# Optimization experiments

Measured on AMD Instinct MI355X. Metric: run time of the kernel, lower is better.

Reference implementation:

```python
import jax, jax.numpy as jnp
import numpy as np

N = 16384
B = 64
VOCAB = 100
L0 = 128
RADIUS = 8.0
BOX = 50.0


def setup_inputs() -> dict:
    key = jax.random.key(0)
    ks = jax.random.split(key, 8)
    z = jax.random.randint(ks[0], (N,), 0, VOCAB, dtype=jnp.int32)
    batch = jnp.sort(jax.random.randint(ks[1], (N,), 0, B, dtype=jnp.int64))
    pos = jax.random.uniform(ks[2], (N, 3), dtype=jnp.float32) * BOX
    emb = jax.random.normal(ks[3], (VOCAB, L0), dtype=jnp.float32)
    w1 = jax.random.normal(ks[4], (L0, 64), dtype=jnp.float32) * (1.0 / np.sqrt(L0))
    b1 = jnp.zeros((64,), dtype=jnp.float32)
    w2 = jax.random.normal(ks[5], (64, 1), dtype=jnp.float32) * (1.0 / 8.0)
    b2 = jnp.zeros((1,), dtype=jnp.float32)
    return {"z": z, "batch": batch, "pos": pos, "emb": emb,
            "w1": w1, "b1": b1, "w2": w2, "b2": b2}


def _radius_graph_mask(pos, batch, r):
    # Brute-force radius graph (what torch_cluster does without grid binning):
    # pairwise squared distances, thresholded, same-graph, no self-loops.
    # Returns a dense [N, N] bool adjacency mask (fixed shape, jit-friendly).
    sq = jnp.sum(pos * pos, axis=-1)                       # [N]
    d2 = sq[:, None] + sq[None, :] - 2.0 * (pos @ pos.T)   # [N, N]
    same_graph = batch[:, None] == batch[None, :]
    not_self = ~jnp.eye(pos.shape[0], dtype=bool)
    return (d2 < r * r) & same_graph & not_self


def reference(z, batch, pos, emb, w1, b1, w2, b2):
    nodes = emb[z]                                         # [N, L0] embedding lookup
    adj = _radius_graph_mask(pos, batch, RADIUS)           # [N, N] bool
    h = jax.nn.silu(nodes @ w1 + b1)                       # [N, 64]
    out = h @ w2 + b2                                      # [N, 1]
    return out, adj
```

## Files before the change

kernel.cpp:

```cpp
#include <hip/hip_runtime.h>
#include <hip/hip_bf16.h>
#include <math.h>

#define N_NODES 16384
#define TI 64
#define TJ 1024

typedef float vf4 __attribute__((ext_vector_type(4)));

__global__ __launch_bounds__(256) void mlp_kernel(const int* __restrict__ z,
                                                  const float* __restrict__ emb,
                                                  const float* __restrict__ w1,
                                                  const float* __restrict__ b1,
                                                  const float* __restrict__ w2,
                                                  const float* __restrict__ b2,
                                                  const int* __restrict__ batch32,
                                                  int* __restrict__ flag,
                                                  float* __restrict__ out) {
    if (blockIdx.x == 0) {
        __shared__ int dec;
        if (threadIdx.x == 0) dec = 0;
        __syncthreads();
        int local = 0;
        for (int k = threadIdx.x; k < N_NODES - 1; k += 256)
            if (batch32[k + 1] < batch32[k]) local = 1;
        if (local) atomicOr(&dec, 1);
        __syncthreads();
        if (threadIdx.x == 0) flag[0] = dec;
    }

    const int lane = threadIdx.x & 63;
    const int wave = threadIdx.x >> 6;
    const int i = blockIdx.x * 4 + wave;
    if (i >= N_NODES) return;

    const float4* erow = (const float4*)(emb + (size_t)z[i] * 128);
    float acc = b1[lane];
#pragma unroll 8
    for (int k4 = 0; k4 < 32; k4++) {
        float4 e = erow[k4];
        int k = k4 * 4;
        acc = fmaf(e.x, w1[(k + 0) * 64 + lane], acc);
        acc = fmaf(e.y, w1[(k + 1) * 64 + lane], acc);
        acc = fmaf(e.z, w1[(k + 2) * 64 + lane], acc);
        acc = fmaf(e.w, w1[(k + 3) * 64 + lane], acc);
    }
    float h = acc / (1.0f + expf(-acc));
    float t = h * w2[lane];
#pragma unroll
    for (int off = 32; off >= 1; off >>= 1)
        t += __shfl_xor(t, off, 64);
    if (lane == 0) out[i] = t + b2[0];
}

template <bool DIAG>
__device__ __forceinline__ void adj_rows(const vf4* __restrict__ s_p,
                                         const int* __restrict__ s_b,
                                         const float xj[4], const float yj[4],
                                         const float zj[4], const float sqj[4],
                                         const int bj[4],
                                         int ibase, int j0,
                                         float* __restrict__ orow) {
#pragma unroll 4
    for (int ii = 0; ii < TI; ii++) {
        vf4 p = s_p[ii];
        const float xi = p.x, yi = p.y, zi = p.z, sqi = p.w;
        const int bi = s_b[ii];
        float r[4];
#pragma unroll
        for (int m = 0; m < 4; m++) {
            float dot = fmaf(zi, zj[m], fmaf(yi, yj[m], __fmul_rn(xi, xj[m])));
            float d2 = __fsub_rn(__fadd_rn(sqi, sqj[m]), __fadd_rn(dot, dot));
            bool v = (d2 < 64.0f) && (bi == bj[m]);
            if (DIAG) v = v && ((ibase + ii) != (j0 + m));
            r[m] = v ? 1.0f : 0.0f;
        }
        vf4 rv = {r[0], r[1], r[2], r[3]};
        __builtin_nontemporal_store(rv, (vf4*)(orow + (size_t)ii * N_NODES));
    }
}

__global__ __launch_bounds__(256) void adj_kernel(const float* __restrict__ pos,
                                                  const void* __restrict__ batch_raw,
                                                  const int* __restrict__ flag,
                                                  float* __restrict__ adj) {
    __shared__ vf4 s_p[TI];
    __shared__ int s_b[TI];

    const bool is64 = (flag[0] != 0);
    const int* b32 = (const int*)batch_raw;
    const long long* b64 = (const long long*)batch_raw;

    const int t     = threadIdx.x;
    const int jbase = blockIdx.x * TJ;
    const int ibase = blockIdx.y * TI;
    const int j0    = jbase + t * 4;
    float* orow = adj + (size_t)ibase * N_NODES + j0;

    int b_lo, b_hi, c_lo, c_hi;
    if (is64) {
        b_lo = (int)b64[ibase];  b_hi = (int)b64[ibase + TI - 1];
        c_lo = (int)b64[jbase];  c_hi = (int)b64[jbase + TJ - 1];
    } else {
        b_lo = b32[ibase];  b_hi = b32[ibase + TI - 1];
        c_lo = b32[jbase];  c_hi = b32[jbase + TJ - 1];
    }

    if (b_hi < c_lo || c_hi < b_lo) {
        vf4 zero = {0.0f, 0.0f, 0.0f, 0.0f};
#pragma unroll 8
        for (int ii = 0; ii < TI; ii++)
            __builtin_nontemporal_store(zero, (vf4*)(orow + (size_t)ii * N_NODES));
        return;
    }

    if (t < TI) {
        int i = ibase + t;
        float x = pos[i * 3 + 0], y = pos[i * 3 + 1], z = pos[i * 3 + 2];
        vf4 p;
        p.x = x; p.y = y; p.z = z;
        p.w = __fadd_rn(__fadd_rn(__fmul_rn(x, x), __fmul_rn(y, y)), __fmul_rn(z, z));
        s_p[t] = p;
        s_b[t] = is64 ? (int)b64[i] : b32[i];
    }
    __syncthreads();

    const float4* p4 = (const float4*)(pos + (size_t)jbase * 3);
    float4 A = p4[t * 3 + 0];
    float4 B = p4[t * 3 + 1];
    float4 C = p4[t * 3 + 2];
    const float xj[4] = {A.x, A.w, B.z, C.y};
    const float yj[4] = {A.y, B.x, B.w, C.z};
    const float zj[4] = {A.z, B.y, C.x, C.w};

    float sqj[4];
#pragma unroll
    for (int m = 0; m < 4; m++)
        sqj[m] = __fadd_rn(__fadd_rn(__fmul_rn(xj[m], xj[m]), __fmul_rn(yj[m], yj[m])),
                           __fmul_rn(zj[m], zj[m]));

    int bj[4];
    if (is64) {
#pragma unroll
        for (int m = 0; m < 4; m++) bj[m] = (int)b64[j0 + m];
    } else {
        int4 bb = *(const int4*)(b32 + j0);
        bj[0] = bb.x; bj[1] = bb.y; bj[2] = bb.z; bj[3] = bb.w;
    }

    if ((unsigned)(ibase - jbase) < (unsigned)TJ)
        adj_rows<true>(s_p, s_b, xj, yj, zj, sqj, bj, ibase, j0, orow);
    else
        adj_rows<false>(s_p, s_b, xj, yj, zj, sqj, bj, ibase, j0, orow);
}

extern "C" void kernel_launch(void* const* d_in, const int* in_sizes, int n_in,
                              void* d_out, int out_size, void* d_ws, size_t ws_size,
                              hipStream_t stream) {
    const int*   z     = (const int*)d_in[0];
    const void*  batch = d_in[1];
    const float* pos   = (const float*)d_in[2];
    const float* emb   = (const float*)d_in[3];
    const float* w1    = (const float*)d_in[4];
    const float* b1    = (const float*)d_in[5];
    const float* w2    = (const float*)d_in[6];
    const float* b2    = (const float*)d_in[7];

    float* out = (float*)d_out;
    float* adj = out + N_NODES;
    int* flag = (int*)d_ws;

    mlp_kernel<<<N_NODES / 4, 256, 0, stream>>>(z, emb, w1, b1, w2, b2,
                                                (const int*)batch, flag, out);
    adj_kernel<<<dim3(N_NODES / TJ, N_NODES / TI), 256, 0, stream>>>(pos, batch, flag, adj);
}
```

Baseline: 1.120 ms.

## Compute graph segment bounds via binary search and restrict adjacency compute to them

Block 0 of the MLP kernel now also binary-searches the sorted batch array for each graph's start offset and writes these to the workspace. The adjacency kernel switches to row-strip blocks of 8 rows. Each block computes distances only over the column range of its graphs and writes plain zero stores elsewhere. This drops the distance and compare work for cross-graph columns, at the cost of smaller row tiles with less reuse of column positions per load and a variable per-block workload.

```diff
diff --git a/kernel.cpp b/kernel.cpp
--- a/kernel.cpp
+++ b/kernel.cpp
@@ -1,10 +1,9 @@
 #include <hip/hip_runtime.h>
-#include <hip/hip_bf16.h>
 #include <math.h>
 
 #define N_NODES 16384
-#define TI 64
-#define TJ 1024
+#define TI 8
+#define NCH (N_NODES / 4)
 
 typedef float vf4 __attribute__((ext_vector_type(4)));
 
@@ -15,7 +14,7 @@
                                                   const float* __restrict__ w2,
                                                   const float* __restrict__ b2,
                                                   const int* __restrict__ batch32,
-                                                  int* __restrict__ flag,
+                                                  int* __restrict__ ws,
                                                   float* __restrict__ out) {
     if (blockIdx.x == 0) {
         __shared__ int dec;
@@ -26,7 +25,19 @@
             if (batch32[k + 1] < batch32[k]) local = 1;
         if (local) atomicOr(&dec, 1);
         __syncthreads();
-        if (threadIdx.x == 0) flag[0] = dec;
+        const bool is64 = (dec != 0);
+        const long long* b64v = (const long long*)batch32;
+        if (threadIdx.x < 65) {
+            const int v = threadIdx.x;
+            int lo = 0, hi = N_NODES;
+            while (lo < hi) {
+                int mid = (lo + hi) >> 1;
+                int bm = is64 ? (int)b64v[mid] : batch32[mid];
+                if (bm < v) lo = mid + 1; else hi = mid;
+            }
+            ws[1 + v] = lo;
+        }
+        if (threadIdx.x == 0) ws[0] = dec;
     }
 
     const int lane = threadIdx.x & 63;
@@ -53,69 +64,30 @@
     if (lane == 0) out[i] = t + b2[0];
 }
 
-template <bool DIAG>
-__device__ __forceinline__ void adj_rows(const vf4* __restrict__ s_p,
-                                         const int* __restrict__ s_b,
-                                         const float xj[4], const float yj[4],
-                                         const float zj[4], const float sqj[4],
-                                         const int bj[4],
-                                         int ibase, int j0,
-                                         float* __restrict__ orow) {
-#pragma unroll 4
-    for (int ii = 0; ii < TI; ii++) {
-        vf4 p = s_p[ii];
-        const float xi = p.x, yi = p.y, zi = p.z, sqi = p.w;
-        const int bi = s_b[ii];
-        float r[4];
-#pragma unroll
-        for (int m = 0; m < 4; m++) {
-            float dot = fmaf(zi, zj[m], fmaf(yi, yj[m], __fmul_rn(xi, xj[m])));
-            float d2 = __fsub_rn(__fadd_rn(sqi, sqj[m]), __fadd_rn(dot, dot));
-            bool v = (d2 < 64.0f) && (bi == bj[m]);
-            if (DIAG) v = v && ((ibase + ii) != (j0 + m));
-            r[m] = v ? 1.0f : 0.0f;
-        }
-        vf4 rv = {r[0], r[1], r[2], r[3]};
-        __builtin_nontemporal_store(rv, (vf4*)(orow + (size_t)ii * N_NODES));
-    }
-}
-
 __global__ __launch_bounds__(256) void adj_kernel(const float* __restrict__ pos,
                                                   const void* __restrict__ batch_raw,
-                                                  const int* __restrict__ flag,
+                                                  const int* __restrict__ ws,
                                                   float* __restrict__ adj) {
     __shared__ vf4 s_p[TI];
     __shared__ int s_b[TI];
 
-    const bool is64 = (flag[0] != 0);
+    const bool is64 = (ws[0] != 0);
     const int* b32 = (const int*)batch_raw;
     const long long* b64 = (const long long*)batch_raw;
 
-    const int t     = threadIdx.x;
-    const int jbase = blockIdx.x * TJ;
-    const int ibase = blockIdx.y * TI;
-    const int j0    = jbase + t * 4;
-    float* orow = adj + (size_t)ibase * N_NODES + j0;
+    const int t  = threadIdx.x;
+    const int i0 = blockIdx.x * TI;
 
-    int b_lo, b_hi, c_lo, c_hi;
-    if (is64) {
-        b_lo = (int)b64[ibase];  b_hi = (int)b64[ibase + TI - 1];
-        c_lo = (int)b64[jbase];  c_hi = (int)b64[jbase + TJ - 1];
-    } else {
-        b_lo = b32[ibase];  b_hi = b32[ibase + TI - 1];
-        c_lo = b32[jbase];  c_hi = b32[jbase + TJ - 1];
-    }
+    const int b_lo = is64 ? (int)b64[i0] : b32[i0];
+    const int b_hi = is64 ? (int)b64[i0 + TI - 1] : b32[i0 + TI - 1];
 
-    if (b_hi < c_lo || c_hi < b_lo) {
-        vf4 zero = {0.0f, 0.0f, 0.0f, 0.0f};
-#pragma unroll 8
-        for (int ii = 0; ii < TI; ii++)
-            __builtin_nontemporal_store(zero, (vf4*)(orow + (size_t)ii * N_NODES));
-        return;
-    }
+    const int jlo = ws[1 + b_lo];
+    const int jhi = ws[2 + b_hi];
+    const int clo = jlo >> 2;
+    const int chi = (jhi + 3) >> 2;
 
     if (t < TI) {
-        int i = ibase + t;
+        const int i = i0 + t;
         float x = pos[i * 3 + 0], y = pos[i * 3 + 1], z = pos[i * 3 + 2];
         vf4 p;
         p.x = x; p.y = y; p.z = z;
@@ -125,33 +97,58 @@
     }
     __syncthreads();
 
-    const float4* p4 = (const float4*)(pos + (size_t)jbase * 3);
-    float4 A = p4[t * 3 + 0];
-    float4 B = p4[t * 3 + 1];
-    float4 C = p4[t * 3 + 2];
-    const float xj[4] = {A.x, A.w, B.z, C.y};
-    const float yj[4] = {A.y, B.x, B.w, C.z};
-    const float zj[4] = {A.z, B.y, C.x, C.w};
-
-    float sqj[4];
+    const vf4 zero = {0.0f, 0.0f, 0.0f, 0.0f};
 #pragma unroll
-    for (int m = 0; m < 4; m++)
-        sqj[m] = __fadd_rn(__fadd_rn(__fmul_rn(xj[m], xj[m]), __fmul_rn(yj[m], yj[m])),
-                           __fmul_rn(zj[m], zj[m]));
-
-    int bj[4];
-    if (is64) {
-#pragma unroll
-        for (int m = 0; m < 4; m++) bj[m] = (int)b64[j0 + m];
-    } else {
-        int4 bb = *(const int4*)(b32 + j0);
-        bj[0] = bb.x; bj[1] = bb.y; bj[2] = bb.z; bj[3] = bb.w;
+    for (int r = 0; r < TI; r++) {
+        vf4* row4 = (vf4*)(adj + (size_t)(i0 + r) * N_NODES);
+        for (int c = t; c < clo; c += 256)
+            __builtin_nontemporal_store(zero, row4 + c);
+        for (int c = chi + t; c < NCH; c += 256)
+            __builtin_nontemporal_store(zero, row4 + c);
     }
 
-    if ((unsigned)(ibase - jbase) < (unsigned)TJ)
-        adj_rows<true>(s_p, s_b, xj, yj, zj, sqj, bj, ibase, j0, orow);
-    else
-        adj_rows<false>(s_p, s_b, xj, yj, zj, sqj, bj, ibase, j0, orow);
+    for (int c = clo + t; c < chi; c += 256) {
+        const int j0 = c * 4;
+        const float4* p4 = (const float4*)pos;
+        float4 A = p4[c * 3 + 0];
+        float4 B = p4[c * 3 + 1];
+        float4 C = p4[c * 3 + 2];
+        const float xj[4] = {A.x, A.w, B.z, C.y};
+        const float yj[4] = {A.y, B.x, B.w, C.z};
+        const float zj[4] = {A.z, B.y, C.x, C.w};
+
+        float sqj[4];
+#pragma unroll
+        for (int m = 0; m < 4; m++)
+            sqj[m] = __fadd_rn(__fadd_rn(__fmul_rn(xj[m], xj[m]), __fmul_rn(yj[m], yj[m])),
+                               __fmul_rn(zj[m], zj[m]));
+
+        int bj[4];
+        if (is64) {
+#pragma unroll
+            for (int m = 0; m < 4; m++) bj[m] = (int)b64[j0 + m];
+        } else {
+            int4 bb = *(const int4*)(b32 + j0);
+            bj[0] = bb.x; bj[1] = bb.y; bj[2] = bb.z; bj[3] = bb.w;
+        }
+
+#pragma unroll
+        for (int r = 0; r < TI; r++) {
+            vf4 p = s_p[r];
+            const float xi = p.x, yi = p.y, zi = p.z, sqi = p.w;
+            const int bi = s_b[r];
+            float rr[4];
+#pragma unroll
+            for (int m = 0; m < 4; m++) {
+                float dot = fmaf(zi, zj[m], fmaf(yi, yj[m], __fmul_rn(xi, xj[m])));
+                float d2 = __fsub_rn(__fadd_rn(sqi, sqj[m]), __fadd_rn(dot, dot));
+                bool v = (d2 < 64.0f) && (bi == bj[m]) && ((i0 + r) != (j0 + m));
+                rr[m] = v ? 1.0f : 0.0f;
+            }
+            vf4 rv = {rr[0], rr[1], rr[2], rr[3]};
+            __builtin_nontemporal_store(rv, (vf4*)(adj + (size_t)(i0 + r) * N_NODES + j0));
+        }
+    }
 }
 
 extern "C" void kernel_launch(void* const* d_in, const int* in_sizes, int n_in,
@@ -168,9 +165,9 @@
 
     float* out = (float*)d_out;
     float* adj = out + N_NODES;
-    int* flag = (int*)d_ws;
+    int* ws = (int*)d_ws;
 
     mlp_kernel<<<N_NODES / 4, 256, 0, stream>>>(z, emb, w1, b1, w2, b2,
-                                                (const int*)batch, flag, out);
-    adj_kernel<<<dim3(N_NODES / TJ, N_NODES / TI), 256, 0, stream>>>(pos, batch, flag, adj);
+                                                (const int*)batch, ws, out);
+    adj_kernel<<<N_NODES / TI, 256, 0, stream>>>(pos, batch, ws, adj);
 }
```

Result: slower. 1.144 ms (+2.1%).
